# Kernel optimization log

Measured on AMD Instinct MI355X. Metric: run time of the kernel, lower is better.

Reference implementation:

```python
import jax, jax.numpy as jnp
import numpy as np

MAX_DISP = 48


def setup_inputs() -> dict:
    key = jax.random.key(0)
    k1, k2 = jax.random.split(key)
    b, c, h, w = 8, 128, 96, 320
    left_feature = jax.random.normal(k1, (b, c, h, w), dtype=jnp.float32)
    right_feature = jax.random.normal(k2, (b, c, h, w), dtype=jnp.float32)
    return {"left_feature": left_feature, "right_feature": right_feature}


def reference(left_feature, right_feature):
    # Correlation cost volume: cost[b, i, h, x] = mean_c left[b,c,h,x] * right[b,c,h,x-i]
    # for x >= i, zero elsewhere. Loop is over the fixed disparity count (48),
    # each iteration touching only the valid width slice (honors the sparsity
    # structure of the original; no [b,c,h,D,w] intermediate is materialized).
    b, c, h, w = left_feature.shape
    slices = []
    for i in range(MAX_DISP):
        if i > 0:
            corr = (left_feature[:, :, :, i:] * right_feature[:, :, :, : w - i]).mean(axis=1)
            corr = jnp.pad(corr, ((0, 0), (0, 0), (i, 0)))  # zeros for x < i
        else:
            corr = (left_feature * right_feature).mean(axis=1)
        slices.append(corr)
    return jnp.stack(slices, axis=1)  # (b, max_disp, h, w)
```

## Files before the change

kernel.cpp:

```cpp
#include <hip/hip_runtime.h>
#include <stdint.h>


typedef __bf16 bf16x8 __attribute__((ext_vector_type(8)));
typedef short short8v __attribute__((ext_vector_type(8)));
typedef float floatx16 __attribute__((ext_vector_type(16)));

constexpr int W = 320, H = 96, C = 128, NB = 8, MAXD = 48;
constexpr int HW = H * W;
constexpr int KC = 32;

__device__ __forceinline__ uint32_t pack_bf16x2(float a, float b) {
    uint32_t ua = __float_as_uint(a), ub = __float_as_uint(b);
    uint32_t lo = (ua + 0x7fffu + ((ua >> 16) & 1u)) >> 16;
    uint32_t hi = (ub + 0x7fffu + ((ub >> 16) & 1u)) & 0xffff0000u;
    return hi | lo;
}

__global__ __launch_bounds__(640, 5) void cost_volume_kernel(
    const float* __restrict__ Lg, const float* __restrict__ Rg,
    float* __restrict__ out)
{
    __shared__ uint32_t lds[15840];
    ushort* sL = reinterpret_cast<ushort*>(lds);
    ushort* sR = sL + KC * W;

    const int t    = threadIdx.x;
    const int lane = t & 63;
    const int p    = t >> 6;
    const int n    = lane & 31;
    const int half = lane >> 5;

    const int b = blockIdx.x / H;
    const int h = blockIdx.x % H;
    const int baseLR = b * (C * HW) + h * W;

    floatx16 acc0 = 0.f, acc1 = 0.f, acc2 = 0.f;

    for (int c0 = 0; c0 < C; c0 += KC) {
#pragma unroll
        for (int j = 0; j < 4; ++j) {
            int idx = j * 640 + t;
            int row = idx / 80;
            int col = (idx % 80) * 4;
            int g = baseLR + (c0 + row) * HW + col;
            float4 vl = *reinterpret_cast<const float4*>(Lg + g);
            float4 vr = *reinterpret_cast<const float4*>(Rg + g);
            uint32_t* dl = reinterpret_cast<uint32_t*>(sL + row * W + col);
            dl[0] = pack_bf16x2(vl.x, vl.y);
            dl[1] = pack_bf16x2(vl.z, vl.w);
            uint32_t* dr = reinterpret_cast<uint32_t*>(sR + row * W + col);
            dr[0] = pack_bf16x2(vr.x, vr.y);
            dr[1] = pack_bf16x2(vr.z, vr.w);
        }
        __syncthreads();

#pragma unroll
        for (int ks = 0; ks < 2; ++ks) {
            const int kb = ks * 16 + half * 8;
            const ushort* pa = sL + kb * W + p * 32 + n;
            short8v av;
#pragma unroll
            for (int j = 0; j < 8; ++j) av[j] = (short)pa[j * W];
            bf16x8 af = __builtin_bit_cast(bf16x8, av);

            {
                const ushort* pb = sR + kb * W + p * 32 + n;
                short8v bv;
#pragma unroll
                for (int j = 0; j < 8; ++j) bv[j] = (short)pb[j * W];
                acc0 = __builtin_amdgcn_mfma_f32_32x32x16_bf16(
                    af, __builtin_bit_cast(bf16x8, bv), acc0, 0, 0, 0);
            }
            if (p >= 1) {
                const ushort* pb = sR + kb * W + (p - 1) * 32 + n;
                short8v bv;
#pragma unroll
                for (int j = 0; j < 8; ++j) bv[j] = (short)pb[j * W];
                acc1 = __builtin_amdgcn_mfma_f32_32x32x16_bf16(
                    af, __builtin_bit_cast(bf16x8, bv), acc1, 0, 0, 0);
            }
            if (p >= 2) {
                const ushort* pb = sR + kb * W + (p - 2) * 32 + n;
                short8v bv;
#pragma unroll
                for (int j = 0; j < 8; ++j) bv[j] = (short)pb[j * W];
                acc2 = __builtin_amdgcn_mfma_f32_32x32x16_bf16(
                    af, __builtin_bit_cast(bf16x8, bv), acc2, 0, 0, 0);
            }
        }
        __syncthreads();
    }

    float* sS = reinterpret_cast<float*>(lds) + p * (MAXD * 33);

    if (p < 2) {
        for (int e = lane; e < MAXD * 33; e += 64) sS[e] = 0.f;
    }

#define FILL_TILE(DP, ACC)                                                  \
    if (p >= (DP)) {                                                        \
        _Pragma("unroll")                                                   \
        for (int r = 0; r < 16; ++r) {                                      \
            int m = (r & 3) + 8 * (r >> 2) + 4 * half;                      \
            int i = 32 * (DP) + m - n;                                      \
            if (i >= 0 && i < MAXD)                                         \
                sS[i * 33 + m] = ACC[r] * (1.f / 128.f);                    \
        }                                                                   \
    }
    FILL_TILE(0, acc0)
    FILL_TILE(1, acc1)
    FILL_TILE(2, acc2)
#undef FILL_TILE

    const int ob = b * (MAXD * HW) + h * W + p * 32;
#pragma unroll
    for (int e = 0; e < 24; ++e) {
        int idx = e * 64 + lane;
        int i = idx >> 5;
        int m = idx & 31;
        out[ob + i * HW + m] = sS[i * 33 + m];
    }
}

extern "C" void kernel_launch(void* const* d_in, const int* in_sizes, int n_in,
                              void* d_out, int out_size, void* d_ws, size_t ws_size,
                              hipStream_t stream) {
    const float* L = (const float*)d_in[0];
    const float* R = (const float*)d_in[1];
    float* out = (float*)d_out;
    cost_volume_kernel<<<dim3(NB * H), dim3(640), 0, stream>>>(L, R, out);
}
```

Measured before the change: 288.1 us.

## Prefetch next channel chunk into registers, pack channel pairs, and shrink the LDS footprint

Global loads for the next 32-channel chunk are issued into registers right after the barrier, so they overlap the MFMA work on the current chunk. Shared memory now stores adjacent channel pairs packed into 32-bit words, so each MFMA operand is read with four 32-bit loads instead of eight 16-bit loads. The epilogue writes the 48 disparities in three 16-row passes, which cuts the shared buffer from about 63KB to 40KB and should allow more blocks per CU. Output writes use nontemporal stores. The cost is more live registers for the prefetched float4 values, which can put pressure on the launch bound of 5.

Result: slower. 425.7 us (+47.7%).

```diff
diff --git a/kernel.cpp b/kernel.cpp
--- a/kernel.cpp
+++ b/kernel.cpp
@@ -3,12 +3,13 @@
 
 
 typedef __bf16 bf16x8 __attribute__((ext_vector_type(8)));
-typedef short short8v __attribute__((ext_vector_type(8)));
 typedef float floatx16 __attribute__((ext_vector_type(16)));
 
 constexpr int W = 320, H = 96, C = 128, NB = 8, MAXD = 48;
 constexpr int HW = H * W;
 constexpr int KC = 32;
+constexpr int CP = KC / 2;
+constexpr int MATD = CP * W;
 
 __device__ __forceinline__ uint32_t pack_bf16x2(float a, float b) {
     uint32_t ua = __float_as_uint(a), ub = __float_as_uint(b);
@@ -21,9 +22,7 @@
     const float* __restrict__ Lg, const float* __restrict__ Rg,
     float* __restrict__ out)
 {
-    __shared__ uint32_t lds[15840];
-    ushort* sL = reinterpret_cast<ushort*>(lds);
-    ushort* sR = sL + KC * W;
+    __shared__ uint32_t lds[2 * MATD];
 
     const int t    = threadIdx.x;
     const int lane = t & 63;
@@ -35,91 +34,131 @@
     const int h = blockIdx.x % H;
     const int baseLR = b * (C * HW) + h * W;
 
+    const int rp = t / 80;
+    const int c4 = t % 80;
+    const int goff = 2 * rp * HW + 4 * c4;
+    uint32_t* dstL = lds + rp * W + 4 * c4;
+    uint32_t* dstR = dstL + MATD;
+
+    float4 la0, la1, lb0, lb1, ra0, ra1, rb0, rb1;
+
+    auto loadChunk = [&](int c0) {
+        const float* Lp = Lg + baseLR + c0 * HW + goff;
+        const float* Rp = Rg + baseLR + c0 * HW + goff;
+        la0 = *(const float4*)(Lp);
+        la1 = *(const float4*)(Lp + HW);
+        lb0 = *(const float4*)(Lp + 16 * HW);
+        lb1 = *(const float4*)(Lp + 17 * HW);
+        ra0 = *(const float4*)(Rp);
+        ra1 = *(const float4*)(Rp + HW);
+        rb0 = *(const float4*)(Rp + 16 * HW);
+        rb1 = *(const float4*)(Rp + 17 * HW);
+    };
+
+    auto writeLDS = [&]() {
+        uint4 v;
+        v.x = pack_bf16x2(la0.x, la1.x);
+        v.y = pack_bf16x2(la0.y, la1.y);
+        v.z = pack_bf16x2(la0.z, la1.z);
+        v.w = pack_bf16x2(la0.w, la1.w);
+        *reinterpret_cast<uint4*>(dstL) = v;
+        v.x = pack_bf16x2(lb0.x, lb1.x);
+        v.y = pack_bf16x2(lb0.y, lb1.y);
+        v.z = pack_bf16x2(lb0.z, lb1.z);
+        v.w = pack_bf16x2(lb0.w, lb1.w);
+        *reinterpret_cast<uint4*>(dstL + 8 * W) = v;
+        v.x = pack_bf16x2(ra0.x, ra1.x);
+        v.y = pack_bf16x2(ra0.y, ra1.y);
+        v.z = pack_bf16x2(ra0.z, ra1.z);
+        v.w = pack_bf16x2(ra0.w, ra1.w);
+        *reinterpret_cast<uint4*>(dstR) = v;
+        v.x = pack_bf16x2(rb0.x, rb1.x);
+        v.y = pack_bf16x2(rb0.y, rb1.y);
+        v.z = pack_bf16x2(rb0.z, rb1.z);
+        v.w = pack_bf16x2(rb0.w, rb1.w);
+        *reinterpret_cast<uint4*>(dstR + 8 * W) = v;
+    };
+
     floatx16 acc0 = 0.f, acc1 = 0.f, acc2 = 0.f;
 
-    for (int c0 = 0; c0 < C; c0 += KC) {
+    loadChunk(0);
 #pragma unroll
-        for (int j = 0; j < 4; ++j) {
-            int idx = j * 640 + t;
-            int row = idx / 80;
-            int col = (idx % 80) * 4;
-            int g = baseLR + (c0 + row) * HW + col;
-            float4 vl = *reinterpret_cast<const float4*>(Lg + g);
-            float4 vr = *reinterpret_cast<const float4*>(Rg + g);
-            uint32_t* dl = reinterpret_cast<uint32_t*>(sL + row * W + col);
-            dl[0] = pack_bf16x2(vl.x, vl.y);
-            dl[1] = pack_bf16x2(vl.z, vl.w);
-            uint32_t* dr = reinterpret_cast<uint32_t*>(sR + row * W + col);
-            dr[0] = pack_bf16x2(vr.x, vr.y);
-            dr[1] = pack_bf16x2(vr.z, vr.w);
-        }
+    for (int ck = 0; ck < 4; ++ck) {
+        writeLDS();
         __syncthreads();
+        if (ck < 3) loadChunk((ck + 1) * KC);
 
+        const uint32_t* sL = lds;
+        const uint32_t* sR = lds + MATD;
 #pragma unroll
         for (int ks = 0; ks < 2; ++ks) {
-            const int kb = ks * 16 + half * 8;
-            const ushort* pa = sL + kb * W + p * 32 + n;
-            short8v av;
-#pragma unroll
-            for (int j = 0; j < 8; ++j) av[j] = (short)pa[j * W];
-            bf16x8 af = __builtin_bit_cast(bf16x8, av);
+            const int pr = ks * 8 + half * 4;
+            const uint32_t* pa = sL + pr * W + p * 32 + n;
+            uint4 a4;
+            a4.x = pa[0 * W]; a4.y = pa[1 * W]; a4.z = pa[2 * W]; a4.w = pa[3 * W];
+            bf16x8 af = __builtin_bit_cast(bf16x8, a4);
 
             {
-                const ushort* pb = sR + kb * W + p * 32 + n;
-                short8v bv;
-#pragma unroll
-                for (int j = 0; j < 8; ++j) bv[j] = (short)pb[j * W];
+                const uint32_t* pb = sR + pr * W + p * 32 + n;
+                uint4 b4;
+                b4.x = pb[0 * W]; b4.y = pb[1 * W]; b4.z = pb[2 * W]; b4.w = pb[3 * W];
                 acc0 = __builtin_amdgcn_mfma_f32_32x32x16_bf16(
-                    af, __builtin_bit_cast(bf16x8, bv), acc0, 0, 0, 0);
+                    af, __builtin_bit_cast(bf16x8, b4), acc0, 0, 0, 0);
             }
             if (p >= 1) {
-                const ushort* pb = sR + kb * W + (p - 1) * 32 + n;
-                short8v bv;
-#pragma unroll
-                for (int j = 0; j < 8; ++j) bv[j] = (short)pb[j * W];
+                const uint32_t* pb = sR + pr * W + (p - 1) * 32 + n;
+                uint4 b4;
+                b4.x = pb[0 * W]; b4.y = pb[1 * W]; b4.z = pb[2 * W]; b4.w = pb[3 * W];
                 acc1 = __builtin_amdgcn_mfma_f32_32x32x16_bf16(
-                    af, __builtin_bit_cast(bf16x8, bv), acc1, 0, 0, 0);
+                    af, __builtin_bit_cast(bf16x8, b4), acc1, 0, 0, 0);
             }
             if (p >= 2) {
-                const ushort* pb = sR + kb * W + (p - 2) * 32 + n;
-                short8v bv;
-#pragma unroll
-                for (int j = 0; j < 8; ++j) bv[j] = (short)pb[j * W];
+                const uint32_t* pb = sR + pr * W + (p - 2) * 32 + n;
+                uint4 b4;
+                b4.x = pb[0 * W]; b4.y = pb[1 * W]; b4.z = pb[2 * W]; b4.w = pb[3 * W];
                 acc2 = __builtin_amdgcn_mfma_f32_32x32x16_bf16(
-                    af, __builtin_bit_cast(bf16x8, bv), acc2, 0, 0, 0);
+                    af, __builtin_bit_cast(bf16x8, b4), acc2, 0, 0, 0);
             }
         }
         __syncthreads();
     }
 
-    float* sS = reinterpret_cast<float*>(lds) + p * (MAXD * 33);
+    float* sS = reinterpret_cast<float*>(lds) + p * (16 * 33);
+    const int ob = b * (MAXD * HW) + h * W + p * 32;
+    constexpr float scale = 1.f / 128.f;
 
-    if (p < 2) {
-        for (int e = lane; e < MAXD * 33; e += 64) sS[e] = 0.f;
-    }
-
+#pragma unroll
+    for (int pass = 0; pass < 3; ++pass) {
+        const int r0 = pass * 16;
+        if (p < 2) {
+#pragma unroll
+            for (int e = 0; e < 9; ++e) {
+                int idx = e * 64 + lane;
+                if (idx < 16 * 33) sS[idx] = 0.f;
+            }
+        }
 #define FILL_TILE(DP, ACC)                                                  \
-    if (p >= (DP)) {                                                        \
-        _Pragma("unroll")                                                   \
-        for (int r = 0; r < 16; ++r) {                                      \
-            int m = (r & 3) + 8 * (r >> 2) + 4 * half;                      \
-            int i = 32 * (DP) + m - n;                                      \
-            if (i >= 0 && i < MAXD)                                         \
-                sS[i * 33 + m] = ACC[r] * (1.f / 128.f);                    \
-        }                                                                   \
-    }
-    FILL_TILE(0, acc0)
-    FILL_TILE(1, acc1)
-    FILL_TILE(2, acc2)
+        if (p >= (DP)) {                                                    \
+            _Pragma("unroll")                                               \
+            for (int r = 0; r < 16; ++r) {                                  \
+                int m = (r & 3) + 8 * (r >> 2) + 4 * half;                  \
+                int i = 32 * (DP) + m - n;                                  \
+                if (i >= r0 && i < r0 + 16)                                 \
+                    sS[(i - r0) * 33 + m] = ACC[r] * scale;                 \
+            }                                                               \
+        }
+        FILL_TILE(0, acc0)
+        FILL_TILE(1, acc1)
+        FILL_TILE(2, acc2)
 #undef FILL_TILE
-
-    const int ob = b * (MAXD * HW) + h * W + p * 32;
 #pragma unroll
-    for (int e = 0; e < 24; ++e) {
-        int idx = e * 64 + lane;
-        int i = idx >> 5;
-        int m = idx & 31;
-        out[ob + i * HW + m] = sS[i * 33 + m];
+        for (int e = 0; e < 8; ++e) {
+            int idx = e * 64 + lane;
+            int ii = idx >> 5;
+            int m  = idx & 31;
+            __builtin_nontemporal_store(sS[ii * 33 + m],
+                                        &out[ob + (r0 + ii) * HW + m]);
+        }
     }
 }
 
```
